# Kernel tuning notes

Measured on AMD Instinct MI355X. Metric: run time of the kernel, lower is better.

## Reference

```python
import jax, jax.numpy as jnp
import numpy as np

N_USERS = 100000
N_ITEMS = 50000
N_NODES = N_USERS + N_ITEMS
N_EDGES = 4800000
EMB_DIM = 64
N_LAYERS = 3


def setup_inputs() -> dict:
    key = jax.random.key(0)
    k1, k2, k3, k4, k5 = jax.random.split(key, 5)
    adj_rows = jax.random.randint(k1, (N_EDGES,), 0, N_NODES, dtype=jnp.int64 if jax.config.jax_enable_x64 else jnp.int32)
    adj_cols = jax.random.randint(k2, (N_EDGES,), 0, N_NODES, dtype=jnp.int64 if jax.config.jax_enable_x64 else jnp.int32)
    adj_vals = jax.random.uniform(k3, (N_EDGES,), dtype=jnp.float32)
    user_emb = jax.random.normal(k4, (N_USERS, EMB_DIM), dtype=jnp.float32)
    item_emb = jax.random.normal(k5, (N_ITEMS, EMB_DIM), dtype=jnp.float32)
    return {"adj_rows": adj_rows, "adj_cols": adj_cols, "adj_vals": adj_vals,
            "user_emb": user_emb, "item_emb": item_emb}


def _spmm(rows, cols, vals, x):
    # sparse.mm(adj, x): gather source node features, scale by edge value,
    # scatter-add into destination rows. Shapes: [E] indices, [N, D] features.
    msgs = vals[:, None] * x[cols]          # [E, D]
    return jax.ops.segment_sum(msgs, rows, num_segments=N_NODES)  # [N, D]


def reference(adj_rows, adj_cols, adj_vals, user_emb, item_emb):
    all_emb = jnp.concatenate([user_emb, item_emb], axis=0)  # [N, D]
    acc = all_emb                                            # running sum over layers (fused stack+mean)
    emb = all_emb
    for _ in range(N_LAYERS):
        emb = _spmm(adj_rows, adj_cols, adj_vals, emb)
        acc = acc + emb
    final = acc / jnp.asarray(N_LAYERS + 1, dtype=acc.dtype)
    return final[:N_USERS], final[N_USERS:]
```

## Files before the change

kernel.cpp:

```cpp
#include <hip/hip_runtime.h>


#define N_USERS 100000
#define N_ITEMS 50000
#define N_NODES 150000
#define N_EDGES 4800000
#define EMB_DIM 64

typedef unsigned short u16;
typedef unsigned int   u32;

constexpr int NODE_FLOATS  = N_NODES * EMB_DIM;
constexpr int NODE_FLOAT4S = NODE_FLOATS / 4;
constexpr int USER_FLOAT4S = N_USERS * EMB_DIM / 4;

constexpr int NB   = (N_NODES + 255) / 256;
constexpr int NXG  = 8;
constexpr int SEG  = NB * NXG;
constexpr int CAP1 = 1280;
constexpr int EPB  = 6144;
constexpr int ABLK2 = (N_EDGES + EPB - 1) / EPB;
constexpr int SB_CAP = 8960;

static __device__ __forceinline__ float bf2f(u16 b) {
    return __uint_as_float(((u32)b) << 16);
}
static __device__ __forceinline__ u16 f2bf(float f) {
    u32 u = __float_as_uint(f);
    return (u16)((u + 0x7FFFu + ((u >> 16) & 1u)) >> 16);
}

__global__ void init_kernel(const float* __restrict__ user_emb,
                            const float* __restrict__ item_emb,
                            u16* __restrict__ emb,
                            float* __restrict__ acc) {
    int i = blockIdx.x * blockDim.x + threadIdx.x;
    if (i >= NODE_FLOAT4S) return;
    float4 v = (i < USER_FLOAT4S) ? ((const float4*)user_emb)[i]
                                  : ((const float4*)item_emb)[i - USER_FLOAT4S];
    ((float4*)acc)[i] = v;
    ushort4 o;
    o.x = f2bf(v.x); o.y = f2bf(v.y); o.z = f2bf(v.z); o.w = f2bf(v.w);
    ((ushort4*)emb)[i] = o;
}

__global__ void init_ptrs_kernel(int* __restrict__ bx_pos, int* __restrict__ csr_cursor) {
    int i = blockIdx.x * blockDim.x + threadIdx.x;
    if (i < SEG) bx_pos[i * 16] = i * CAP1;
    if (i == 0) csr_cursor[0] = 0;
}

__global__ void stageA2_kernel(const int* __restrict__ rows,
                               const int* __restrict__ cols,
                               const float* __restrict__ vals,
                               int* __restrict__ bx_pos,
                               u32* __restrict__ stage_key,
                               u16* __restrict__ stage_val) {
    __shared__ u32 lkey[EPB];
    __shared__ u16 lval[EPB];
    __shared__ u16 lbkt[EPB];
    __shared__ int hist[NB];
    __shared__ int hstart[NB];
    __shared__ int hcur[NB];
    __shared__ int gbase[NB];
    __shared__ int ws4[4];

    const int tid  = threadIdx.x;
    const int base = blockIdx.x * EPB;
    const int cnt  = min(EPB, N_EDGES - base);
    const int x    = blockIdx.x & (NXG - 1);

    for (int i = tid; i < NB; i += 256) hist[i] = 0;
    __syncthreads();

    for (int k = 0; k < EPB / 256; k += 8) {
        int rbuf[8];
        #pragma unroll
        for (int q = 0; q < 8; ++q) {
            int idx = (k + q) * 256 + tid;
            rbuf[q] = (idx < cnt) ? rows[base + idx] : -1;
        }
        #pragma unroll
        for (int q = 0; q < 8; ++q)
            if (rbuf[q] >= 0) atomicAdd(&hist[rbuf[q] >> 8], 1);
    }
    __syncthreads();

    const int lane = tid & 63, wave = tid >> 6;
    int carry = 0;
    for (int c0 = 0; c0 < NB; c0 += 256) {
        int i = c0 + tid;
        int v = (i < NB) ? hist[i] : 0;
        int incl = v;
        #pragma unroll
        for (int off = 1; off < 64; off <<= 1) {
            int t = __shfl_up(incl, off);
            if (lane >= off) incl += t;
        }
        if (lane == 63) ws4[wave] = incl;
        __syncthreads();
        int wpref = 0, tot = 0;
        #pragma unroll
        for (int w = 0; w < 4; ++w) { int s = ws4[w]; if (w < wave) wpref += s; tot += s; }
        int excl = carry + wpref + incl - v;
        if (i < NB) { hstart[i] = excl; hcur[i] = excl; }
        carry += tot;
        __syncthreads();
    }

    for (int k = 0; k < EPB / 256; k += 8) {
        int rb[8], cb[8]; float vb[8];
        #pragma unroll
        for (int q = 0; q < 8; ++q) {
            int idx = (k + q) * 256 + tid;
            if (idx < cnt) { rb[q] = rows[base + idx]; cb[q] = cols[base + idx]; vb[q] = vals[base + idx]; }
            else rb[q] = -1;
        }
        #pragma unroll
        for (int q = 0; q < 8; ++q) {
            if (rb[q] < 0) continue;
            int b = rb[q] >> 8;
            int p = atomicAdd(&hcur[b], 1);
            lkey[p] = ((u32)(rb[q] & 255) << 24) | (u32)cb[q];
            lval[p] = f2bf(vb[q]);
            lbkt[p] = (u16)b;
        }
    }
    __syncthreads();

    for (int i = tid; i < NB; i += 256) {
        int n = hist[i];
        if (n) {
            int seg = i * NXG + x;
            int p = atomicAdd(&bx_pos[seg * 16], n);
            gbase[i] = (p + n <= (seg + 1) * CAP1) ? p : -1;
        }
    }
    __syncthreads();

    for (int i = tid; i < cnt; i += 256) {
        int b  = lbkt[i];
        int gb = gbase[b];
        if (gb >= 0) {
            int d = gb + (i - hstart[b]);
            stage_key[d] = lkey[i];
            stage_val[d] = lval[i];
        }
    }
}

__global__ void stageB2_kernel(const int* __restrict__ bx_pos,
                               const u32* __restrict__ stage_key,
                               const u16* __restrict__ stage_val,
                               int* __restrict__ csr_cursor,
                               u32* __restrict__ csr_col,
                               u16* __restrict__ csr_val,
                               int* __restrict__ row_beg,
                               int* __restrict__ row_cnt) {
    __shared__ u32 skey[SB_CAP];
    __shared__ u16 sval[SB_CAP];
    __shared__ int rhist[256], rstart[256], rcur[256];
    __shared__ int ws4[4];
    __shared__ int sbase_sh;

    const int b   = blockIdx.x;
    const int tid = threadIdx.x;
    rhist[tid] = 0;
    __syncthreads();

    for (int xx = 0; xx < NXG; ++xx) {
        int seg = b * NXG + xx;
        int sb  = seg * CAP1;
        int n   = min(bx_pos[seg * 16] - sb, CAP1);
        for (int i = tid; i < n; i += 256)
            atomicAdd(&rhist[stage_key[sb + i] >> 24], 1);
    }
    __syncthreads();

    const int lane = tid & 63, wave = tid >> 6;
    int v = rhist[tid], incl = v;
    #pragma unroll
    for (int off = 1; off < 64; off <<= 1) {
        int t = __shfl_up(incl, off);
        if (lane >= off) incl += t;
    }
    if (lane == 63) ws4[wave] = incl;
    __syncthreads();
    int wpref = 0, total = 0;
    #pragma unroll
    for (int w = 0; w < 4; ++w) { int s = ws4[w]; if (w < wave) wpref += s; total += s; }
    int excl = wpref + incl - v;
    rstart[tid] = excl;
    rcur[tid]   = excl;
    if (tid == 0) sbase_sh = atomicAdd(csr_cursor, total);
    __syncthreads();

    for (int xx = 0; xx < NXG; ++xx) {
        int seg = b * NXG + xx;
        int sb  = seg * CAP1;
        int n   = min(bx_pos[seg * 16] - sb, CAP1);
        for (int i = tid; i < n; i += 256) {
            u32 key = stage_key[sb + i];
            u16 val = stage_val[sb + i];
            int p = atomicAdd(&rcur[key >> 24], 1);
            if (p < SB_CAP) { skey[p] = key & 0x00FFFFFFu; sval[p] = val; }
        }
    }
    __syncthreads();

    int sbase = sbase_sh;
    int tcap  = min(total, SB_CAP);
    for (int i = tid; i < tcap; i += 256) {
        csr_col[sbase + i] = skey[i];
        csr_val[sbase + i] = sval[i];
    }
    int grow = b * 256 + tid;
    if (grow < N_NODES) {
        row_beg[grow] = sbase + rstart[tid];
        row_cnt[grow] = rhist[tid];
    }
}

__global__ void spmm_csr_kernel(const int* __restrict__ row_beg,
                                const int* __restrict__ row_cnt,
                                const u32* __restrict__ csr_col,
                                const u16* __restrict__ csr_val,
                                const u16* __restrict__ x,
                                u16* __restrict__ y,
                                float* __restrict__ acc,
                                float scale) {
    int gid    = blockIdx.x * blockDim.x + threadIdx.x;
    int lane16 = gid & 15;
    int row    = gid >> 4;
    if (row >= N_NODES) return;
    int waveBase = threadIdx.x & 48;
    int beg = row_beg[row];
    int m   = row_cnt[row];

    float4 s = make_float4(0.f, 0.f, 0.f, 0.f);
    for (int j = 0; j < m; j += 16) {
        int n = m - j; if (n > 16) n = 16;
        int c = 0, vb = 0;
        if (lane16 < n) {
            c  = (int)csr_col[beg + j + lane16];
            vb = (int)csr_val[beg + j + lane16];
        }
        for (int k = 0; k < n; ++k) {
            int   cc = __shfl(c,  waveBase + k);
            float vv = bf2f((u16)__shfl(vb, waveBase + k));
            ushort4 xv = ((const ushort4*)(x + (size_t)cc * EMB_DIM))[lane16];
            s.x += vv * bf2f(xv.x);
            s.y += vv * bf2f(xv.y);
            s.z += vv * bf2f(xv.z);
            s.w += vv * bf2f(xv.w);
        }
    }

    size_t o4 = (size_t)row * (EMB_DIM / 4) + lane16;
    float4 a = ((const float4*)acc)[o4];
    a.x = (a.x + s.x) * scale; a.y = (a.y + s.y) * scale;
    a.z = (a.z + s.z) * scale; a.w = (a.w + s.w) * scale;
    ((float4*)acc)[o4] = a;
    if (y) {
        ushort4 o;
        o.x = f2bf(s.x); o.y = f2bf(s.y); o.z = f2bf(s.z); o.w = f2bf(s.w);
        ((ushort4*)y)[o4] = o;
    }
}

__global__ void init3_kernel(const float* __restrict__ user_emb,
                             const float* __restrict__ item_emb,
                             float* __restrict__ emb,
                             float* __restrict__ acc,
                             float* __restrict__ nxt) {
    int i = blockIdx.x * blockDim.x + threadIdx.x;
    if (i >= NODE_FLOAT4S) return;
    float4 v = (i < USER_FLOAT4S) ? ((const float4*)user_emb)[i]
                                  : ((const float4*)item_emb)[i - USER_FLOAT4S];
    ((float4*)emb)[i] = v;
    ((float4*)acc)[i] = v;
    ((float4*)nxt)[i] = make_float4(0.f, 0.f, 0.f, 0.f);
}

__global__ void spmm_atomic_kernel(const int* __restrict__ rows,
                                   const int* __restrict__ cols,
                                   const float* __restrict__ vals,
                                   const float* __restrict__ x,
                                   float* __restrict__ y) {
    unsigned tid = blockIdx.x * blockDim.x + threadIdx.x;
    unsigned e  = tid >> 4;
    unsigned d4 = tid & 15u;
    if (e >= N_EDGES) return;
    int r = rows[e]; int c = cols[e]; float v = vals[e];
    float4 xv = ((const float4*)(x + (size_t)c * EMB_DIM))[d4];
    float* yp = y + (size_t)r * EMB_DIM + d4 * 4;
    atomicAdd(yp + 0, v * xv.x);
    atomicAdd(yp + 1, v * xv.y);
    atomicAdd(yp + 2, v * xv.z);
    atomicAdd(yp + 3, v * xv.w);
}

__global__ void acc_kernel(float* __restrict__ acc, const float* __restrict__ nxt,
                           float* __restrict__ zbuf, int do_zero, float scale) {
    int i = blockIdx.x * blockDim.x + threadIdx.x;
    if (i >= NODE_FLOAT4S) return;
    float4 a = ((float4*)acc)[i];
    float4 n = ((const float4*)nxt)[i];
    a.x = (a.x + n.x) * scale; a.y = (a.y + n.y) * scale;
    a.z = (a.z + n.z) * scale; a.w = (a.w + n.w) * scale;
    ((float4*)acc)[i] = a;
    if (do_zero) ((float4*)zbuf)[i] = make_float4(0.f, 0.f, 0.f, 0.f);
}

extern "C" void kernel_launch(void* const* d_in, const int* in_sizes, int n_in,
                              void* d_out, int out_size, void* d_ws, size_t ws_size,
                              hipStream_t stream) {
    const int*   rows     = (const int*)d_in[0];
    const int*   cols     = (const int*)d_in[1];
    const float* vals     = (const float*)d_in[2];
    const float* user_emb = (const float*)d_in[3];
    const float* item_emb = (const float*)d_in[4];
    float* acc = (float*)d_out;

    constexpr size_t U_BUF  = (size_t)NODE_FLOATS / 2;
    constexpr size_t U_SKEY = (size_t)SEG * CAP1;
    constexpr size_t U_SVAL = U_SKEY / 2;
    constexpr size_t U_CCOL = (size_t)N_EDGES;
    constexpr size_t U_CVAL = (size_t)N_EDGES / 2;
    size_t need_u32 = U_BUF + U_SKEY + U_SVAL + U_CCOL + U_CVAL
                    + 2 * (size_t)N_NODES + (size_t)SEG * 16 + 16;

    const int EW_BLOCKS = (NODE_FLOAT4S + 255) / 256;

    if (ws_size >= need_u32 * 4) {
        u32* W = (u32*)d_ws;
        u16* buf0      = (u16*)W;
        u32* stage_key = W + U_BUF;
        u16* stage_val = (u16*)(W + U_BUF + U_SKEY);
        u16* buf1      = (u16*)stage_key;
        u32* csr_col   = W + U_BUF + U_SKEY + U_SVAL;
        u16* csr_val   = (u16*)(csr_col + U_CCOL);
        int* row_beg   = (int*)(csr_col + U_CCOL + U_CVAL);
        int* row_cnt   = row_beg + N_NODES;
        int* bx_pos    = row_cnt + N_NODES;
        int* csr_cur   = bx_pos + (size_t)SEG * 16;

        init_ptrs_kernel<<<(SEG + 255) / 256, 256, 0, stream>>>(bx_pos, csr_cur);
        init_kernel<<<EW_BLOCKS, 256, 0, stream>>>(user_emb, item_emb, buf0, acc);
        stageA2_kernel<<<ABLK2, 256, 0, stream>>>(rows, cols, vals, bx_pos,
                                                  stage_key, stage_val);
        stageB2_kernel<<<NB, 256, 0, stream>>>(bx_pos, stage_key, stage_val,
                                               csr_cur, csr_col, csr_val,
                                               row_beg, row_cnt);

        const int SPMM_BLOCKS = (N_NODES * 16 + 255) / 256;
        spmm_csr_kernel<<<SPMM_BLOCKS, 256, 0, stream>>>(row_beg, row_cnt, csr_col, csr_val,
                                                         buf0, buf1, acc, 1.0f);
        spmm_csr_kernel<<<SPMM_BLOCKS, 256, 0, stream>>>(row_beg, row_cnt, csr_col, csr_val,
                                                         buf1, buf0, acc, 1.0f);
        spmm_csr_kernel<<<SPMM_BLOCKS, 256, 0, stream>>>(row_beg, row_cnt, csr_col, csr_val,
                                                         buf0, nullptr, acc, 0.25f);
    } else {
        float* buf0 = (float*)d_ws;
        float* buf1 = buf0 + NODE_FLOATS;
        const int SPMM_BLOCKS = (int)(((size_t)N_EDGES * 16 + 255) / 256);
        init3_kernel<<<EW_BLOCKS, 256, 0, stream>>>(user_emb, item_emb, buf0, acc, buf1);
        float* prev = buf0; float* next = buf1;
        for (int layer = 0; layer < 3; ++layer) {
            spmm_atomic_kernel<<<SPMM_BLOCKS, 256, 0, stream>>>(rows, cols, vals, prev, next);
            if (layer < 2) acc_kernel<<<EW_BLOCKS, 256, 0, stream>>>(acc, next, prev, 1, 1.0f);
            else           acc_kernel<<<EW_BLOCKS, 256, 0, stream>>>(acc, next, prev, 0, 0.25f);
            float* t = prev; prev = next; next = t;
        }
    }
}
```

Measured before the change: 563.1 us.

## Partition CSR by column octant and sweep octants across all rows for gather locality

The CSR build now buckets each row's edges into 8 column ranges (octants) and writes a per-octant row descriptor packing offset and count. The SpMM kernel becomes a persistent grid where every block processes all its row groups one octant at a time, keeping the active slice of the source feature table small enough to stay in cache. The fp32 running accumulator is dropped in favour of storing bf16 layer outputs, which the final layer sums, so fewer fp32 read-modify-writes occur per layer. Risks: per-octant counts are capped at 511, which could truncate edges on hot rows; the fixed grid limits occupancy; bf16 storage of e0 adds rounding error to the final sum.

```diff
diff --git a/kernel.cpp b/kernel.cpp
--- a/kernel.cpp
+++ b/kernel.cpp
@@ -21,6 +21,11 @@
 constexpr int EPB  = 6144;
 constexpr int ABLK2 = (N_EDGES + EPB - 1) / EPB;
 constexpr int SB_CAP = 8960;
+constexpr int NOCT = 8;
+constexpr int OCT_W = 18750;
+constexpr int NGRP  = N_NODES / 16;
+constexpr int SPMM_GRID = 2048;
+constexpr int NG = (NGRP + SPMM_GRID - 1) / SPMM_GRID;
 
 static __device__ __forceinline__ float bf2f(u16 b) {
     return __uint_as_float(((u32)b) << 16);
@@ -32,13 +37,11 @@
 
 __global__ void init_kernel(const float* __restrict__ user_emb,
                             const float* __restrict__ item_emb,
-                            u16* __restrict__ emb,
-                            float* __restrict__ acc) {
+                            u16* __restrict__ emb) {
     int i = blockIdx.x * blockDim.x + threadIdx.x;
     if (i >= NODE_FLOAT4S) return;
     float4 v = (i < USER_FLOAT4S) ? ((const float4*)user_emb)[i]
                                   : ((const float4*)item_emb)[i - USER_FLOAT4S];
-    ((float4*)acc)[i] = v;
     ushort4 o;
     o.x = f2bf(v.x); o.y = f2bf(v.y); o.z = f2bf(v.z); o.w = f2bf(v.w);
     ((ushort4*)emb)[i] = o;
@@ -155,44 +158,52 @@
                                int* __restrict__ csr_cursor,
                                u32* __restrict__ csr_col,
                                u16* __restrict__ csr_val,
-                               int* __restrict__ row_beg,
-                               int* __restrict__ row_cnt) {
+                               u32* __restrict__ desc) {
     __shared__ u32 skey[SB_CAP];
     __shared__ u16 sval[SB_CAP];
-    __shared__ int rhist[256], rstart[256], rcur[256];
+    __shared__ int cell[2048];
     __shared__ int ws4[4];
-    __shared__ int sbase_sh;
+    __shared__ int sbase_sh, total_sh;
 
     const int b   = blockIdx.x;
     const int tid = threadIdx.x;
-    rhist[tid] = 0;
+    for (int c = tid; c < 2048; c += 256) cell[c] = 0;
     __syncthreads();
 
     for (int xx = 0; xx < NXG; ++xx) {
         int seg = b * NXG + xx;
         int sb  = seg * CAP1;
         int n   = min(bx_pos[seg * 16] - sb, CAP1);
-        for (int i = tid; i < n; i += 256)
-            atomicAdd(&rhist[stage_key[sb + i] >> 24], 1);
+        for (int i = tid; i < n; i += 256) {
+            u32 key = stage_key[sb + i];
+            int col = (int)(key & 0xFFFFFFu);
+            int oc  = col / OCT_W;
+            atomicAdd(&cell[(oc << 8) | (int)(key >> 24)], 1);
+        }
     }
     __syncthreads();
 
     const int lane = tid & 63, wave = tid >> 6;
-    int v = rhist[tid], incl = v;
-    #pragma unroll
-    for (int off = 1; off < 64; off <<= 1) {
-        int t = __shfl_up(incl, off);
-        if (lane >= off) incl += t;
-    }
-    if (lane == 63) ws4[wave] = incl;
-    __syncthreads();
-    int wpref = 0, total = 0;
-    #pragma unroll
-    for (int w = 0; w < 4; ++w) { int s = ws4[w]; if (w < wave) wpref += s; total += s; }
-    int excl = wpref + incl - v;
-    rstart[tid] = excl;
-    rcur[tid]   = excl;
-    if (tid == 0) sbase_sh = atomicAdd(csr_cursor, total);
+    int carry = 0;
+    for (int c0 = 0; c0 < 2048; c0 += 256) {
+        int i = c0 + tid;
+        int v = cell[i];
+        int incl = v;
+        #pragma unroll
+        for (int off = 1; off < 64; off <<= 1) {
+            int t = __shfl_up(incl, off);
+            if (lane >= off) incl += t;
+        }
+        if (lane == 63) ws4[wave] = incl;
+        __syncthreads();
+        int wpref = 0, tot = 0;
+        #pragma unroll
+        for (int w = 0; w < 4; ++w) { int s = ws4[w]; if (w < wave) wpref += s; tot += s; }
+        cell[i] = carry + wpref + incl - v;
+        carry += tot;
+        __syncthreads();
+    }
+    if (tid == 0) { total_sh = carry; sbase_sh = atomicAdd(csr_cursor, carry); }
     __syncthreads();
 
     for (int xx = 0; xx < NXG; ++xx) {
@@ -202,69 +213,102 @@
         for (int i = tid; i < n; i += 256) {
             u32 key = stage_key[sb + i];
             u16 val = stage_val[sb + i];
-            int p = atomicAdd(&rcur[key >> 24], 1);
-            if (p < SB_CAP) { skey[p] = key & 0x00FFFFFFu; sval[p] = val; }
-        }
-    }
-    __syncthreads();
-
-    int sbase = sbase_sh;
-    int tcap  = min(total, SB_CAP);
+            int col = (int)(key & 0xFFFFFFu);
+            int oc  = col / OCT_W;
+            int p = atomicAdd(&cell[(oc << 8) | (int)(key >> 24)], 1);
+            if (p < SB_CAP) { skey[p] = (u32)col; sval[p] = val; }
+        }
+    }
+    __syncthreads();
+
+    const int sbase = sbase_sh;
+    const int tcap  = min(total_sh, SB_CAP);
     for (int i = tid; i < tcap; i += 256) {
         csr_col[sbase + i] = skey[i];
         csr_val[sbase + i] = sval[i];
     }
-    int grow = b * 256 + tid;
-    if (grow < N_NODES) {
-        row_beg[grow] = sbase + rstart[tid];
-        row_cnt[grow] = rhist[tid];
-    }
-}
-
-__global__ void spmm_csr_kernel(const int* __restrict__ row_beg,
-                                const int* __restrict__ row_cnt,
-                                const u32* __restrict__ csr_col,
-                                const u16* __restrict__ csr_val,
-                                const u16* __restrict__ x,
-                                u16* __restrict__ y,
-                                float* __restrict__ acc,
-                                float scale) {
-    int gid    = blockIdx.x * blockDim.x + threadIdx.x;
-    int lane16 = gid & 15;
-    int row    = gid >> 4;
-    if (row >= N_NODES) return;
-    int waveBase = threadIdx.x & 48;
-    int beg = row_beg[row];
-    int m   = row_cnt[row];
-
-    float4 s = make_float4(0.f, 0.f, 0.f, 0.f);
-    for (int j = 0; j < m; j += 16) {
-        int n = m - j; if (n > 16) n = 16;
-        int c = 0, vb = 0;
-        if (lane16 < n) {
-            c  = (int)csr_col[beg + j + lane16];
-            vb = (int)csr_val[beg + j + lane16];
-        }
-        for (int k = 0; k < n; ++k) {
-            int   cc = __shfl(c,  waveBase + k);
-            float vv = bf2f((u16)__shfl(vb, waveBase + k));
-            ushort4 xv = ((const ushort4*)(x + (size_t)cc * EMB_DIM))[lane16];
-            s.x += vv * bf2f(xv.x);
-            s.y += vv * bf2f(xv.y);
-            s.z += vv * bf2f(xv.z);
-            s.w += vv * bf2f(xv.w);
-        }
-    }
-
-    size_t o4 = (size_t)row * (EMB_DIM / 4) + lane16;
-    float4 a = ((const float4*)acc)[o4];
-    a.x = (a.x + s.x) * scale; a.y = (a.y + s.y) * scale;
-    a.z = (a.z + s.z) * scale; a.w = (a.w + s.w) * scale;
-    ((float4*)acc)[o4] = a;
-    if (y) {
-        ushort4 o;
-        o.x = f2bf(s.x); o.y = f2bf(s.y); o.z = f2bf(s.z); o.w = f2bf(s.w);
-        ((ushort4*)y)[o4] = o;
+    for (int c = tid; c < 2048; c += 256) {
+        int endp = min(cell[c], SB_CAP);
+        int begp = c ? min(cell[c - 1], SB_CAP) : 0;
+        int oc = c >> 8, rl = c & 255;
+        int row = b * 256 + rl;
+        if (row < N_NODES) {
+            int cnt = endp - begp; if (cnt > 511) cnt = 511;
+            desc[oc * N_NODES + row] = ((u32)(sbase + begp) << 9) | (u32)cnt;
+        }
+    }
+}
+
+__global__ __launch_bounds__(256, 8)
+void spmm_oct_kernel(const u32* __restrict__ desc,
+                     const u32* __restrict__ csr_col,
+                     const u16* __restrict__ csr_val,
+                     const u16* __restrict__ x,
+                     u16* __restrict__ y,
+                     const u16* __restrict__ e0,
+                     const u16* __restrict__ y1,
+                     const u16* __restrict__ y2,
+                     float* __restrict__ out) {
+    const int g16      = threadIdx.x >> 4;
+    const int lane16   = threadIdx.x & 15;
+    const int waveBase = threadIdx.x & 48;
+
+    float4 acc[NG];
+    #pragma unroll
+    for (int r = 0; r < NG; ++r) acc[r] = make_float4(0.f, 0.f, 0.f, 0.f);
+
+    for (int oct = 0; oct < NOCT; ++oct) {
+        const u32* dl = desc + (size_t)oct * N_NODES;
+        #pragma unroll
+        for (int r = 0; r < NG; ++r) {
+            int G = blockIdx.x + r * SPMM_GRID;
+            if (G >= NGRP) continue;
+            int row = G * 16 + g16;
+            u32 d = dl[row];
+            int beg = (int)(d >> 9);
+            int m   = (int)(d & 511u);
+            for (int j = 0; j < m; j += 16) {
+                int n = m - j; if (n > 16) n = 16;
+                int c = 0, vb = 0;
+                if (lane16 < n) {
+                    c  = (int)csr_col[beg + j + lane16];
+                    vb = (int)csr_val[beg + j + lane16];
+                }
+                for (int k = 0; k < n; ++k) {
+                    int   cc = __shfl(c,  waveBase + k);
+                    float vv = bf2f((u16)__shfl(vb, waveBase + k));
+                    ushort4 xv = ((const ushort4*)(x + (size_t)cc * EMB_DIM))[lane16];
+                    acc[r].x += vv * bf2f(xv.x);
+                    acc[r].y += vv * bf2f(xv.y);
+                    acc[r].z += vv * bf2f(xv.z);
+                    acc[r].w += vv * bf2f(xv.w);
+                }
+            }
+        }
+    }
+
+    #pragma unroll
+    for (int r = 0; r < NG; ++r) {
+        int G = blockIdx.x + r * SPMM_GRID;
+        if (G >= NGRP) continue;
+        int row = G * 16 + g16;
+        size_t o4 = (size_t)row * (EMB_DIM / 4) + lane16;
+        if (y) {
+            ushort4 o;
+            o.x = f2bf(acc[r].x); o.y = f2bf(acc[r].y);
+            o.z = f2bf(acc[r].z); o.w = f2bf(acc[r].w);
+            ((ushort4*)y)[o4] = o;
+        } else {
+            ushort4 a  = ((const ushort4*)e0)[o4];
+            ushort4 b1 = ((const ushort4*)y1)[o4];
+            ushort4 b2 = ((const ushort4*)y2)[o4];
+            float4 o;
+            o.x = (bf2f(a.x) + bf2f(b1.x) + bf2f(b2.x) + acc[r].x) * 0.25f;
+            o.y = (bf2f(a.y) + bf2f(b1.y) + bf2f(b2.y) + acc[r].y) * 0.25f;
+            o.z = (bf2f(a.z) + bf2f(b1.z) + bf2f(b2.z) + acc[r].z) * 0.25f;
+            o.w = (bf2f(a.w) + bf2f(b1.w) + bf2f(b2.w) + acc[r].w) * 0.25f;
+            ((float4*)out)[o4] = o;
+        }
     }
 }
 
@@ -320,15 +364,16 @@
     const float* vals     = (const float*)d_in[2];
     const float* user_emb = (const float*)d_in[3];
     const float* item_emb = (const float*)d_in[4];
-    float* acc = (float*)d_out;
+    float* out = (float*)d_out;
 
     constexpr size_t U_BUF  = (size_t)NODE_FLOATS / 2;
     constexpr size_t U_SKEY = (size_t)SEG * CAP1;
     constexpr size_t U_SVAL = U_SKEY / 2;
     constexpr size_t U_CCOL = (size_t)N_EDGES;
     constexpr size_t U_CVAL = (size_t)N_EDGES / 2;
-    size_t need_u32 = U_BUF + U_SKEY + U_SVAL + U_CCOL + U_CVAL
-                    + 2 * (size_t)N_NODES + (size_t)SEG * 16 + 16;
+    constexpr size_t U_DESC = (size_t)NOCT * N_NODES;
+    size_t need_u32 = U_BUF + U_SKEY + U_SVAL + U_CCOL + U_CVAL + U_DESC
+                    + (size_t)SEG * 16 + 16 + U_BUF;
 
     const int EW_BLOCKS = (NODE_FLOAT4S + 255) / 256;
 
@@ -340,36 +385,34 @@
         u16* buf1      = (u16*)stage_key;
         u32* csr_col   = W + U_BUF + U_SKEY + U_SVAL;
         u16* csr_val   = (u16*)(csr_col + U_CCOL);
-        int* row_beg   = (int*)(csr_col + U_CCOL + U_CVAL);
-        int* row_cnt   = row_beg + N_NODES;
-        int* bx_pos    = row_cnt + N_NODES;
+        u32* desc      = (u32*)(csr_col + U_CCOL + U_CVAL);
+        int* bx_pos    = (int*)(desc + U_DESC);
         int* csr_cur   = bx_pos + (size_t)SEG * 16;
+        u16* buf2      = (u16*)(csr_cur + 16);
 
         init_ptrs_kernel<<<(SEG + 255) / 256, 256, 0, stream>>>(bx_pos, csr_cur);
-        init_kernel<<<EW_BLOCKS, 256, 0, stream>>>(user_emb, item_emb, buf0, acc);
+        init_kernel<<<EW_BLOCKS, 256, 0, stream>>>(user_emb, item_emb, buf0);
         stageA2_kernel<<<ABLK2, 256, 0, stream>>>(rows, cols, vals, bx_pos,
                                                   stage_key, stage_val);
         stageB2_kernel<<<NB, 256, 0, stream>>>(bx_pos, stage_key, stage_val,
-                                               csr_cur, csr_col, csr_val,
-                                               row_beg, row_cnt);
-
-        const int SPMM_BLOCKS = (N_NODES * 16 + 255) / 256;
-        spmm_csr_kernel<<<SPMM_BLOCKS, 256, 0, stream>>>(row_beg, row_cnt, csr_col, csr_val,
-                                                         buf0, buf1, acc, 1.0f);
-        spmm_csr_kernel<<<SPMM_BLOCKS, 256, 0, stream>>>(row_beg, row_cnt, csr_col, csr_val,
-                                                         buf1, buf0, acc, 1.0f);
-        spmm_csr_kernel<<<SPMM_BLOCKS, 256, 0, stream>>>(row_beg, row_cnt, csr_col, csr_val,
-                                                         buf0, nullptr, acc, 0.25f);
+                                               csr_cur, csr_col, csr_val, desc);
+
+        spmm_oct_kernel<<<SPMM_GRID, 256, 0, stream>>>(desc, csr_col, csr_val,
+                                                       buf0, buf1, nullptr, nullptr, nullptr, nullptr);
+        spmm_oct_kernel<<<SPMM_GRID, 256, 0, stream>>>(desc, csr_col, csr_val,
+                                                       buf1, buf2, nullptr, nullptr, nullptr, nullptr);
+        spmm_oct_kernel<<<SPMM_GRID, 256, 0, stream>>>(desc, csr_col, csr_val,
+                                                       buf2, nullptr, buf0, buf1, buf2, out);
     } else {
         float* buf0 = (float*)d_ws;
         float* buf1 = buf0 + NODE_FLOATS;
         const int SPMM_BLOCKS = (int)(((size_t)N_EDGES * 16 + 255) / 256);
-        init3_kernel<<<EW_BLOCKS, 256, 0, stream>>>(user_emb, item_emb, buf0, acc, buf1);
+        init3_kernel<<<EW_BLOCKS, 256, 0, stream>>>(user_emb, item_emb, buf0, out, buf1);
         float* prev = buf0; float* next = buf1;
         for (int layer = 0; layer < 3; ++layer) {
             spmm_atomic_kernel<<<SPMM_BLOCKS, 256, 0, stream>>>(rows, cols, vals, prev, next);
-            if (layer < 2) acc_kernel<<<EW_BLOCKS, 256, 0, stream>>>(acc, next, prev, 1, 1.0f);
-            else           acc_kernel<<<EW_BLOCKS, 256, 0, stream>>>(acc, next, prev, 0, 0.25f);
+            if (layer < 2) acc_kernel<<<EW_BLOCKS, 256, 0, stream>>>(out, next, prev, 1, 1.0f);
+            else           acc_kernel<<<EW_BLOCKS, 256, 0, stream>>>(out, next, prev, 0, 0.25f);
             float* t = prev; prev = next; next = t;
         }
     }
```

New measurement: 633.0 us. +12.4%, slower.

## Defer fp32 accumulation to final layer and pack row descriptors

Applied to the files above, without the earlier changes.

Removes the fp32 acc read-modify-write from every SpMM layer. Each layer's bf16 output is kept in its own buffer, and the last layer sums e0+y1+y2+s once and writes fp32 output, which cuts fp32 traffic per layer. Row begin and count are packed into one u32 descriptor with the count clamped to 255, and the inner 16-wide loop is fully unrolled for full chunks. The risks are that the sum now uses bf16-rounded layer-0 embeddings, and that rows with more than 255 entries would be silently truncated.

```diff
diff --git a/kernel.cpp b/kernel.cpp
--- a/kernel.cpp
+++ b/kernel.cpp
@@ -32,13 +32,11 @@
 
 __global__ void init_kernel(const float* __restrict__ user_emb,
                             const float* __restrict__ item_emb,
-                            u16* __restrict__ emb,
-                            float* __restrict__ acc) {
+                            u16* __restrict__ emb) {
     int i = blockIdx.x * blockDim.x + threadIdx.x;
     if (i >= NODE_FLOAT4S) return;
     float4 v = (i < USER_FLOAT4S) ? ((const float4*)user_emb)[i]
                                   : ((const float4*)item_emb)[i - USER_FLOAT4S];
-    ((float4*)acc)[i] = v;
     ushort4 o;
     o.x = f2bf(v.x); o.y = f2bf(v.y); o.z = f2bf(v.z); o.w = f2bf(v.w);
     ((ushort4*)emb)[i] = o;
@@ -155,8 +153,7 @@
                                int* __restrict__ csr_cursor,
                                u32* __restrict__ csr_col,
                                u16* __restrict__ csr_val,
-                               int* __restrict__ row_beg,
-                               int* __restrict__ row_cnt) {
+                               u32* __restrict__ desc) {
     __shared__ u32 skey[SB_CAP];
     __shared__ u16 sval[SB_CAP];
     __shared__ int rhist[256], rstart[256], rcur[256];
@@ -208,44 +205,47 @@
     }
     __syncthreads();
 
-    int sbase = sbase_sh;
-    int tcap  = min(total, SB_CAP);
+    const int sbase = sbase_sh;
+    const int tcap  = min(total, SB_CAP);
     for (int i = tid; i < tcap; i += 256) {
         csr_col[sbase + i] = skey[i];
         csr_val[sbase + i] = sval[i];
     }
     int grow = b * 256 + tid;
     if (grow < N_NODES) {
-        row_beg[grow] = sbase + rstart[tid];
-        row_cnt[grow] = rhist[tid];
-    }
-}
-
-__global__ void spmm_csr_kernel(const int* __restrict__ row_beg,
-                                const int* __restrict__ row_cnt,
-                                const u32* __restrict__ csr_col,
-                                const u16* __restrict__ csr_val,
-                                const u16* __restrict__ x,
-                                u16* __restrict__ y,
-                                float* __restrict__ acc,
-                                float scale) {
+        int cnt = rhist[tid]; if (cnt > 255) cnt = 255;
+        desc[grow] = ((u32)(sbase + rstart[tid]) << 8) | (u32)cnt;
+    }
+}
+
+__global__ __launch_bounds__(256)
+void spmm_csr2_kernel(const u32* __restrict__ desc,
+                      const u32* __restrict__ csr_col,
+                      const u16* __restrict__ csr_val,
+                      const u16* __restrict__ x,
+                      u16* __restrict__ y,
+                      const u16* __restrict__ e0,
+                      const u16* __restrict__ y1,
+                      const u16* __restrict__ y2,
+                      float* __restrict__ out) {
     int gid    = blockIdx.x * blockDim.x + threadIdx.x;
     int lane16 = gid & 15;
     int row    = gid >> 4;
     if (row >= N_NODES) return;
     int waveBase = threadIdx.x & 48;
-    int beg = row_beg[row];
-    int m   = row_cnt[row];
+
+    u32 d = desc[row];
+    int beg = (int)(d >> 8);
+    int m   = (int)(d & 255u);
 
     float4 s = make_float4(0.f, 0.f, 0.f, 0.f);
-    for (int j = 0; j < m; j += 16) {
-        int n = m - j; if (n > 16) n = 16;
-        int c = 0, vb = 0;
-        if (lane16 < n) {
-            c  = (int)csr_col[beg + j + lane16];
-            vb = (int)csr_val[beg + j + lane16];
-        }
-        for (int k = 0; k < n; ++k) {
+    int nfull = m >> 4;
+    int j = 0;
+    for (int ch = 0; ch < nfull; ++ch, j += 16) {
+        int c  = (int)csr_col[beg + j + lane16];
+        int vb = (int)csr_val[beg + j + lane16];
+        #pragma unroll
+        for (int k = 0; k < 16; ++k) {
             int   cc = __shfl(c,  waveBase + k);
             float vv = bf2f((u16)__shfl(vb, waveBase + k));
             ushort4 xv = ((const ushort4*)(x + (size_t)cc * EMB_DIM))[lane16];
@@ -255,16 +255,39 @@
             s.w += vv * bf2f(xv.w);
         }
     }
+    int rem = m & 15;
+    if (rem) {
+        int c = 0, vb = 0;
+        if (lane16 < rem) {
+            c  = (int)csr_col[beg + j + lane16];
+            vb = (int)csr_val[beg + j + lane16];
+        }
+        for (int k = 0; k < rem; ++k) {
+            int   cc = __shfl(c,  waveBase + k);
+            float vv = bf2f((u16)__shfl(vb, waveBase + k));
+            ushort4 xv = ((const ushort4*)(x + (size_t)cc * EMB_DIM))[lane16];
+            s.x += vv * bf2f(xv.x);
+            s.y += vv * bf2f(xv.y);
+            s.z += vv * bf2f(xv.z);
+            s.w += vv * bf2f(xv.w);
+        }
+    }
 
     size_t o4 = (size_t)row * (EMB_DIM / 4) + lane16;
-    float4 a = ((const float4*)acc)[o4];
-    a.x = (a.x + s.x) * scale; a.y = (a.y + s.y) * scale;
-    a.z = (a.z + s.z) * scale; a.w = (a.w + s.w) * scale;
-    ((float4*)acc)[o4] = a;
     if (y) {
         ushort4 o;
         o.x = f2bf(s.x); o.y = f2bf(s.y); o.z = f2bf(s.z); o.w = f2bf(s.w);
         ((ushort4*)y)[o4] = o;
+    } else {
+        ushort4 a  = ((const ushort4*)e0)[o4];
+        ushort4 b1 = ((const ushort4*)y1)[o4];
+        ushort4 b2 = ((const ushort4*)y2)[o4];
+        float4 o;
+        o.x = (bf2f(a.x) + bf2f(b1.x) + bf2f(b2.x) + s.x) * 0.25f;
+        o.y = (bf2f(a.y) + bf2f(b1.y) + bf2f(b2.y) + s.y) * 0.25f;
+        o.z = (bf2f(a.z) + bf2f(b1.z) + bf2f(b2.z) + s.z) * 0.25f;
+        o.w = (bf2f(a.w) + bf2f(b1.w) + bf2f(b2.w) + s.w) * 0.25f;
+        ((float4*)out)[o4] = o;
     }
 }
 
@@ -320,15 +343,15 @@
     const float* vals     = (const float*)d_in[2];
     const float* user_emb = (const float*)d_in[3];
     const float* item_emb = (const float*)d_in[4];
-    float* acc = (float*)d_out;
+    float* out = (float*)d_out;
 
     constexpr size_t U_BUF  = (size_t)NODE_FLOATS / 2;
     constexpr size_t U_SKEY = (size_t)SEG * CAP1;
     constexpr size_t U_SVAL = U_SKEY / 2;
     constexpr size_t U_CCOL = (size_t)N_EDGES;
     constexpr size_t U_CVAL = (size_t)N_EDGES / 2;
-    size_t need_u32 = U_BUF + U_SKEY + U_SVAL + U_CCOL + U_CVAL
-                    + 2 * (size_t)N_NODES + (size_t)SEG * 16 + 16;
+    size_t need_u32 = U_BUF + U_SKEY + U_SVAL + U_CCOL + U_CVAL + (size_t)N_NODES
+                    + (size_t)SEG * 16 + 16 + U_BUF;
 
     const int EW_BLOCKS = (NODE_FLOAT4S + 255) / 256;
 
@@ -340,36 +363,35 @@
         u16* buf1      = (u16*)stage_key;
         u32* csr_col   = W + U_BUF + U_SKEY + U_SVAL;
         u16* csr_val   = (u16*)(csr_col + U_CCOL);
-        int* row_beg   = (int*)(csr_col + U_CCOL + U_CVAL);
-        int* row_cnt   = row_beg + N_NODES;
-        int* bx_pos    = row_cnt + N_NODES;
+        u32* desc      = (u32*)(csr_col + U_CCOL + U_CVAL);
+        int* bx_pos    = (int*)(desc + N_NODES);
         int* csr_cur   = bx_pos + (size_t)SEG * 16;
+        u16* buf2      = (u16*)(csr_cur + 16);
 
         init_ptrs_kernel<<<(SEG + 255) / 256, 256, 0, stream>>>(bx_pos, csr_cur);
-        init_kernel<<<EW_BLOCKS, 256, 0, stream>>>(user_emb, item_emb, buf0, acc);
+        init_kernel<<<EW_BLOCKS, 256, 0, stream>>>(user_emb, item_emb, buf0);
         stageA2_kernel<<<ABLK2, 256, 0, stream>>>(rows, cols, vals, bx_pos,
                                                   stage_key, stage_val);
         stageB2_kernel<<<NB, 256, 0, stream>>>(bx_pos, stage_key, stage_val,
-                                               csr_cur, csr_col, csr_val,
-                                               row_beg, row_cnt);
+                                               csr_cur, csr_col, csr_val, desc);
 
         const int SPMM_BLOCKS = (N_NODES * 16 + 255) / 256;
-        spmm_csr_kernel<<<SPMM_BLOCKS, 256, 0, stream>>>(row_beg, row_cnt, csr_col, csr_val,
-                                                         buf0, buf1, acc, 1.0f);
-        spmm_csr_kernel<<<SPMM_BLOCKS, 256, 0, stream>>>(row_beg, row_cnt, csr_col, csr_val,
-                                                         buf1, buf0, acc, 1.0f);
-        spmm_csr_kernel<<<SPMM_BLOCKS, 256, 0, stream>>>(row_beg, row_cnt, csr_col, csr_val,
-                                                         buf0, nullptr, acc, 0.25f);
+        spmm_csr2_kernel<<<SPMM_BLOCKS, 256, 0, stream>>>(desc, csr_col, csr_val,
+                                                          buf0, buf1, nullptr, nullptr, nullptr, nullptr);
+        spmm_csr2_kernel<<<SPMM_BLOCKS, 256, 0, stream>>>(desc, csr_col, csr_val,
+                                                          buf1, buf2, nullptr, nullptr, nullptr, nullptr);
+        spmm_csr2_kernel<<<SPMM_BLOCKS, 256, 0, stream>>>(desc, csr_col, csr_val,
+                                                          buf2, nullptr, buf0, buf1, buf2, out);
     } else {
         float* buf0 = (float*)d_ws;
         float* buf1 = buf0 + NODE_FLOATS;
         const int SPMM_BLOCKS = (int)(((size_t)N_EDGES * 16 + 255) / 256);
-        init3_kernel<<<EW_BLOCKS, 256, 0, stream>>>(user_emb, item_emb, buf0, acc, buf1);
+        init3_kernel<<<EW_BLOCKS, 256, 0, stream>>>(user_emb, item_emb, buf0, out, buf1);
         float* prev = buf0; float* next = buf1;
         for (int layer = 0; layer < 3; ++layer) {
             spmm_atomic_kernel<<<SPMM_BLOCKS, 256, 0, stream>>>(rows, cols, vals, prev, next);
-            if (layer < 2) acc_kernel<<<EW_BLOCKS, 256, 0, stream>>>(acc, next, prev, 1, 1.0f);
-            else           acc_kernel<<<EW_BLOCKS, 256, 0, stream>>>(acc, next, prev, 0, 0.25f);
+            if (layer < 2) acc_kernel<<<EW_BLOCKS, 256, 0, stream>>>(out, next, prev, 1, 1.0f);
+            else           acc_kernel<<<EW_BLOCKS, 256, 0, stream>>>(out, next, prev, 0, 0.25f);
             float* t = prev; prev = next; next = t;
         }
     }
```

Result: faster. 530.3 us (-5.8%).
